# Performance work log

Measured on AMD Instinct MI355X. Metric: run time of the kernel, lower is better.

Reference implementation:

```python
import jax, jax.numpy as jnp
import numpy as np

N = 100000      # num_nodes
E = 600000      # edges per relation
R = 3           # num_relations
F_IN = 128
F_OUT = 64


def setup_inputs() -> dict:
    key = jax.random.key(0)
    k0, k1, k2, k3 = jax.random.split(key, 4)
    x = jax.random.normal(k0, (N, F_IN), dtype=jnp.float32)
    edge_indices = jax.random.randint(k1, (R, 2, E), 0, N, dtype=jnp.int32)
    # torch.randperm per relation -> fixed permutations as int inputs
    perms = jnp.stack([jax.random.permutation(jax.random.fold_in(k2, r), N).astype(jnp.int32)
                       for r in range(R)])
    # GCNConv glorot weight + zero bias, one per relation
    Ws = jax.random.normal(k3, (R, F_IN, F_OUT), dtype=jnp.float32) * (1.0 / np.sqrt(F_IN))
    bs = jnp.zeros((R, F_OUT), dtype=jnp.float32)
    return {"x": x, "edge_indices": edge_indices, "perms": perms, "Ws": Ws, "bs": bs}


def gcn_conv(h, src, dst, W, b, n):
    """PyG GCNConv: add self-loops, sym-normalize, linear, scatter-sum, bias."""
    loops = jnp.arange(n, dtype=src.dtype)
    s = jnp.concatenate([src, loops])
    d = jnp.concatenate([dst, loops])
    deg = jax.ops.segment_sum(jnp.ones_like(s, dtype=h.dtype), d, num_segments=n)
    dinv = jnp.where(deg > 0, jax.lax.rsqrt(deg), 0.0)
    norm = dinv[s] * dinv[d]                      # [E+n]
    hw = h @ W                                    # [n, F_OUT]
    out = jax.ops.segment_sum(hw[s] * norm[:, None], d, num_segments=n)
    return out + b


def reference(x, edge_indices, perms, Ws, bs):
    # Eval mode: F.dropout(p=0.5, training=False) is identity.
    n = x.shape[0]
    pos_hs, neg_hs, summaries = [], [], []
    for r in range(R):
        src, dst = edge_indices[r, 0], edge_indices[r, 1]
        pos_h = jax.nn.relu(gcn_conv(x, src, dst, Ws[r], bs[r], n))
        neg_h = jax.nn.relu(gcn_conv(x[perms[r]], src, dst, Ws[r], bs[r], n))
        pos_hs.append(pos_h)
        neg_hs.append(neg_h)
        summaries.append(pos_h.mean(axis=0, keepdims=True))
    return (jnp.stack(pos_hs), jnp.stack(neg_hs), jnp.stack(summaries))
```

## Files before the change

kernel.cpp:

```cpp
#include <hip/hip_runtime.h>

#define F_IN 128
#define F_OUT 64
#define NCHUNK 256

typedef float f32x2 __attribute__((ext_vector_type(2)));
typedef float f32x4 __attribute__((ext_vector_type(4)));
typedef short bf16x8 __attribute__((ext_vector_type(8)));

__device__ __forceinline__ unsigned short f2bf(float f) {
    unsigned int u = __float_as_uint(f);
    u += 0x7fff + ((u >> 16) & 1);
    return (unsigned short)(u >> 16);
}
__device__ __forceinline__ float bf2f(unsigned short s) {
    return __uint_as_float((unsigned int)s << 16);
}

__global__ __launch_bounds__(256) void prep_kernel(const int* __restrict__ ei,
                                                   const int* __restrict__ perm,
                                                   const float* __restrict__ W,
                                                   int* __restrict__ deg,
                                                   int* __restrict__ eoff,
                                                   int* __restrict__ ip,
                                                   unsigned short* __restrict__ wt_hi,
                                                   unsigned short* __restrict__ wt_lo,
                                                   int N, int E, int R,
                                                   int degB, int invB) {
    int b = blockIdx.x;
    if (b < degB) {
        int idx = b * 256 + threadIdx.x;
        if (idx < R * E) {
            int r = idx / E, e = idx - r * E;
            int d = ei[(size_t)r * 2 * E + E + e];
            int pos = atomicAdd(&deg[(size_t)r * N + d], 1);
            eoff[idx] = pos;
        }
    } else if (b < degB + invB) {
        int idx = (b - degB) * 256 + threadIdx.x;
        if (idx < R * N) {
            int r = idx / N, i = idx - r * N;
            ip[(size_t)r * N + perm[idx]] = i;
        }
    } else {
        int idx = (b - degB - invB) * 256 + threadIdx.x;
        if (idx < R * 64 * 128) {
            int k = idx & 127, c = (idx >> 7) & 63, r = idx >> 13;
            float v = W[((size_t)r * F_IN + k) * F_OUT + c];
            unsigned short h = f2bf(v);
            wt_hi[idx] = h;
            wt_lo[idx] = f2bf(v - bf2f(h));
        }
    }
}

__global__ __launch_bounds__(256) void scan_partial(const int* __restrict__ deg,
                                                    int* __restrict__ psum,
                                                    int N, int chunk) {
    int b = blockIdx.x;
    int r = b >> 8, c = b & 255;
    int start = c * chunk, end = min(start + chunk, N);
    int s = 0;
    for (int i = start + threadIdx.x; i < end; i += 256)
        s += deg[(size_t)r * N + i];
    __shared__ int ls[256];
    ls[threadIdx.x] = s;
    __syncthreads();
    for (int off = 128; off > 0; off >>= 1) {
        if (threadIdx.x < off) ls[threadIdx.x] += ls[threadIdx.x + off];
        __syncthreads();
    }
    if (threadIdx.x == 0) psum[b] = ls[0];
}

__global__ __launch_bounds__(256) void scan_apply2(const int* __restrict__ deg,
                                                   const int* __restrict__ psum,
                                                   int* __restrict__ rowstart,
                                                   float* __restrict__ dinv,
                                                   int N, int chunk) {
    int b = blockIdx.x;
    int r = b >> 8, c = b & 255;
    int tid = threadIdx.x, lane = tid & 63, wv = tid >> 6;
    __shared__ int incl[256];
    __shared__ int wsum[4];

    int pv = psum[(r << 8) + tid];
    int sc = pv;
    #pragma unroll
    for (int off = 1; off < 64; off <<= 1) {
        int t = __shfl_up(sc, off, 64);
        if (lane >= off) sc += t;
    }
    if (lane == 63) wsum[wv] = sc;
    __syncthreads();
    int woff = 0;
    for (int w = 0; w < wv; ++w) woff += wsum[w];
    incl[tid] = woff + sc;
    __syncthreads();
    int base = (c == 0) ? 0 : incl[c - 1];
    if (c == 0 && tid == 0)
        rowstart[(size_t)r * (N + 1) + N] = incl[255];

    int start = c * chunk, end = min(start + chunk, N);
    const int* dg = deg + (size_t)r * N;
    int* rs = rowstart + (size_t)r * (N + 1);
    float* dv = dinv + (size_t)r * N;
    int v[4]; int tsum = 0;
    #pragma unroll
    for (int j = 0; j < 4; ++j) {
        int idx = start + tid * 4 + j;
        v[j] = (idx < end) ? dg[idx] : 0;
        tsum += v[j];
    }
    int sc2 = tsum;
    #pragma unroll
    for (int off = 1; off < 64; off <<= 1) {
        int t = __shfl_up(sc2, off, 64);
        if (lane >= off) sc2 += t;
    }
    if (lane == 63) wsum[wv] = sc2;
    __syncthreads();
    int woff2 = 0;
    for (int w = 0; w < wv; ++w) woff2 += wsum[w];
    int excl = base + woff2 + sc2 - tsum;
    #pragma unroll
    for (int j = 0; j < 4; ++j) {
        int idx = start + tid * 4 + j;
        if (idx < end) {
            rs[idx] = excl;
            dv[idx] = rsqrtf((float)(v[j] + 1));
        }
        excl += v[j];
    }
}

__global__ __launch_bounds__(256) void gemm_xw(const float* __restrict__ x,
                                               const unsigned short* __restrict__ wt_hi,
                                               const unsigned short* __restrict__ wt_lo,
                                               const int* __restrict__ ip,
                                               unsigned short* __restrict__ combined,
                                               int N, int R) {
    constexpr int KP = 136;
    __shared__ __align__(16) unsigned short xs_hi[64 * KP];
    __shared__ __align__(16) unsigned short xs_lo[64 * KP];

    int row0 = blockIdx.x * 64;
    int tid = threadIdx.x;
    {
        int rr = tid >> 2, q = tid & 3;
        int grow = row0 + rr; if (grow >= N) grow = N - 1;
        const float* xr = x + (size_t)grow * F_IN + q * 32;
        unsigned short* dh = &xs_hi[rr * KP + q * 32];
        unsigned short* dl = &xs_lo[rr * KP + q * 32];
        #pragma unroll
        for (int c = 0; c < 32; c += 4) {
            float4 v = *(const float4*)(xr + c);
            unsigned short h0 = f2bf(v.x), h1 = f2bf(v.y),
                           h2 = f2bf(v.z), h3 = f2bf(v.w);
            ushort4 hv; hv.x = h0; hv.y = h1; hv.z = h2; hv.w = h3;
            *(ushort4*)(dh + c) = hv;
            ushort4 lv;
            lv.x = f2bf(v.x - bf2f(h0)); lv.y = f2bf(v.y - bf2f(h1));
            lv.z = f2bf(v.z - bf2f(h2)); lv.w = f2bf(v.w - bf2f(h3));
            *(ushort4*)(dl + c) = lv;
        }
    }
    __syncthreads();

    int wv = tid >> 6, lane = tid & 63;
    int l15 = lane & 15, lhi = lane >> 4;
    int nbase = wv * 16;
    for (int r = 0; r < R; ++r) {
        f32x4 acc[4];
        #pragma unroll
        for (int ct = 0; ct < 4; ++ct) acc[ct] = (f32x4){0.f, 0.f, 0.f, 0.f};
        const unsigned short* wh = wt_hi + (size_t)r * 64 * 128;
        const unsigned short* wl = wt_lo + (size_t)r * 64 * 128;
        #pragma unroll
        for (int kc = 0; kc < 4; ++kc) {
            int kb = kc * 32 + lhi * 8;
            int ro = (nbase + l15) * KP + kb;
            bf16x8 bh = *(const bf16x8*)&xs_hi[ro];
            bf16x8 bl = *(const bf16x8*)&xs_lo[ro];
            bf16x8 ah[4], al[4];
            #pragma unroll
            for (int ct = 0; ct < 4; ++ct) {
                int wo = (ct * 16 + l15) * 128 + kb;
                ah[ct] = *(const bf16x8*)(wh + wo);
                al[ct] = *(const bf16x8*)(wl + wo);
            }
            #pragma unroll
            for (int ct = 0; ct < 4; ++ct) {
                acc[ct] = __builtin_amdgcn_mfma_f32_16x16x32_bf16(ah[ct], bh, acc[ct], 0, 0, 0);
                acc[ct] = __builtin_amdgcn_mfma_f32_16x16x32_bf16(ah[ct], bl, acc[ct], 0, 0, 0);
                acc[ct] = __builtin_amdgcn_mfma_f32_16x16x32_bf16(al[ct], bh, acc[ct], 0, 0, 0);
            }
        }
        const int* ipr = ip + (size_t)r * N;
        size_t rb = (size_t)r * N;
        int xrow = row0 + nbase + l15;
        if (xrow < N) {
            int nrow = ipr[xrow];
            #pragma unroll
            for (int ct = 0; ct < 4; ++ct) {
                f32x4 a = acc[ct];
                ushort4 v;
                v.x = f2bf(a.x); v.y = f2bf(a.y);
                v.z = f2bf(a.z); v.w = f2bf(a.w);
                int cb = ct * 16 + lhi * 4;
                *(ushort4*)(combined + (rb + xrow) * 128 + cb) = v;
                *(ushort4*)(combined + (rb + nrow) * 128 + 64 + cb) = v;
            }
        }
    }
}

__global__ __launch_bounds__(256) void fill_csr2(const int* __restrict__ ei,
                                                 const int* __restrict__ eoff,
                                                 const int* __restrict__ rowstart,
                                                 const float* __restrict__ dinv,
                                                 int2* __restrict__ csr,
                                                 int N, int E, int R) {
    int idx = blockIdx.x * 256 + threadIdx.x;
    if (idx >= R * E) return;
    int r = idx / E, e = idx - r * E;
    const int* base = ei + (size_t)r * 2 * E;
    int s = base[e], d = base[E + e];
    const float* dv = dinv + (size_t)r * N;
    float nrm = dv[s] * dv[d];
    int pos = rowstart[(size_t)r * (N + 1) + d] + eoff[idx];
    int2 sp; sp.x = s; sp.y = __float_as_int(nrm);
    csr[(size_t)r * E + pos] = sp;
}

__global__ __launch_bounds__(256) void gather_kernel(const int2* __restrict__ csr,
                                                     const int* __restrict__ rowstart,
                                                     const float* __restrict__ dinv,
                                                     const unsigned short* __restrict__ combined,
                                                     const float* __restrict__ bs,
                                                     float* __restrict__ out_pos,
                                                     float* __restrict__ out_neg,
                                                     float* __restrict__ partial,
                                                     int N, int E, int perRel) {
    int bid = blockIdx.x;
    int r = bid / perRel, ib = bid - r * perRel;
    int lane = threadIdx.x & 63, wv = threadIdx.x >> 6;
    int i = ib * 4 + wv;
    i = __builtin_amdgcn_readfirstlane(i);
    int c0 = (lane & 31) * 2;
    __shared__ float ls[4][64];
    float p0 = 0.f, p1 = 0.f;
    if (i < N) {
        const unsigned short* cw = combined + (size_t)r * N * 128;
        const int* rs = rowstart + (size_t)r * (N + 1);
        int j0 = rs[i], j1 = rs[i + 1];
        j0 = __builtin_amdgcn_readfirstlane(j0);
        j1 = __builtin_amdgcn_readfirstlane(j1);
        float di = dinv[(size_t)r * N + i];
        float w = di * di;
        unsigned int sv = *(const unsigned int*)(cw + (size_t)i * 128 + 2 * lane);
        float acc0 = bf2f((unsigned short)sv) * w;
        float acc1 = bf2f((unsigned short)(sv >> 16)) * w;
        const int2* cs = csr + (size_t)r * E;
        int last = j1 - 1;
        for (int j = j0; j < j1; j += 8) {
            int2 e[8];
            float nm[8];
            #pragma unroll
            for (int k = 0; k < 8; ++k) {
                int idx = j + k;
                int ic = idx < last ? idx : last;
                e[k] = cs[ic];
                nm[k] = (idx < j1) ? __int_as_float(e[k].y) : 0.f;
            }
            #pragma unroll
            for (int k = 0; k < 8; ++k) {
                unsigned int v = *(const unsigned int*)(cw + (size_t)e[k].x * 128 + 2 * lane);
                acc0 += bf2f((unsigned short)v) * nm[k];
                acc1 += bf2f((unsigned short)(v >> 16)) * nm[k];
            }
        }
        float2 bv = *(const float2*)(bs + r * F_OUT + c0);
        float q0 = acc0 + bv.x; q0 = q0 > 0.f ? q0 : 0.f;
        float q1 = acc1 + bv.y; q1 = q1 > 0.f ? q1 : 0.f;
        size_t off = (size_t)r * N * F_OUT + (size_t)i * F_OUT + c0;
        float* dst = (lane < 32) ? (out_pos + off) : (out_neg + off);
        f32x2 o; o.x = q0; o.y = q1;
        __builtin_nontemporal_store(o, (f32x2*)dst);
        if (lane < 32) { p0 = q0; p1 = q1; }
    }
    if (lane < 32) { ls[wv][c0] = p0; ls[wv][c0 + 1] = p1; }
    __syncthreads();
    if (wv == 0) {
        float t = ls[0][lane] + ls[1][lane] + ls[2][lane] + ls[3][lane];
        atomicAdd(&partial[((size_t)r * 256 + (ib & 255)) * F_OUT + lane], t);
    }
}

__global__ __launch_bounds__(256) void summary_reduce(const float* __restrict__ partial,
                                                      float* __restrict__ summary,
                                                      float inv_n) {
    int r = blockIdx.x;
    int lane = threadIdx.x & 63, wv = threadIdx.x >> 6;
    __shared__ float ls[256];
    float s = 0.f;
    for (int c = wv; c < 256; c += 4)
        s += partial[((size_t)r * 256 + c) * F_OUT + lane];
    ls[threadIdx.x] = s;
    __syncthreads();
    if (wv == 0)
        summary[r * F_OUT + lane] =
            (ls[lane] + ls[64 + lane] + ls[128 + lane] + ls[192 + lane]) * inv_n;
}

extern "C" void kernel_launch(void* const* d_in, const int* in_sizes, int n_in,
                              void* d_out, int out_size, void* d_ws, size_t ws_size,
                              hipStream_t stream) {
    const float* x    = (const float*)d_in[0];
    const int*   ei   = (const int*)d_in[1];
    const int*   perm = (const int*)d_in[2];
    const float* Ws   = (const float*)d_in[3];
    const float* bs   = (const float*)d_in[4];

    const int N = in_sizes[0] / F_IN;
    const int R = in_sizes[4] / F_OUT;
    const int E = in_sizes[1] / (2 * R);

    float* out_pos = (float*)d_out;
    float* out_neg = out_pos + (size_t)R * N * F_OUT;
    float* summary = out_neg + (size_t)R * N * F_OUT;

    char* ws = (char*)d_ws;
    size_t off = 0;
    auto alloc = [&](size_t bytes) { void* p = ws + off;
        off += (bytes + 255) & ~(size_t)255; return p; };
    int*   deg      = (int*)  alloc((size_t)R * N * 4);
    float* partial  = (float*)alloc((size_t)R * 256 * F_OUT * 4);
    float* dinv     = (float*)alloc((size_t)R * N * 4);
    int*   rowstart = (int*)  alloc((size_t)R * (N + 1) * 4);
    int*   ip       = (int*)  alloc((size_t)R * N * 4);
    int*   eoff     = (int*)  alloc((size_t)R * E * 4);
    int2*  csr      = (int2*) alloc((size_t)R * E * 8);
    unsigned short* combined = (unsigned short*)alloc((size_t)R * N * 128 * 2);
    int*   psum     = (int*)  alloc((size_t)R * NCHUNK * 4);
    unsigned short* wt_hi = (unsigned short*)alloc((size_t)R * 64 * 128 * 2);
    unsigned short* wt_lo = (unsigned short*)alloc((size_t)R * 64 * 128 * 2);

    const int chunk = (N + NCHUNK - 1) / NCHUNK;
    const int degB = (R * E + 255) / 256;
    const int invB = (R * N + 255) / 256;
    const int wB   = (R * 64 * 128 + 255) / 256;
    const int gemmB = (N + 63) / 64;
    const int perRel = (N + 3) / 4;

    size_t zbytes = (size_t)((char*)dinv - (char*)deg);
    hipMemsetAsync(deg, 0, zbytes, stream);

    prep_kernel<<<degB + invB + wB, 256, 0, stream>>>(ei, perm, Ws, deg, eoff,
                                                      ip, wt_hi, wt_lo, N, E, R,
                                                      degB, invB);
    scan_partial<<<R * NCHUNK, 256, 0, stream>>>(deg, psum, N, chunk);
    scan_apply2<<<R * NCHUNK, 256, 0, stream>>>(deg, psum, rowstart, dinv, N, chunk);
    gemm_xw<<<gemmB, 256, 0, stream>>>(x, wt_hi, wt_lo, ip, combined, N, R);
    fill_csr2<<<(R * E + 255) / 256, 256, 0, stream>>>(ei, eoff, rowstart, dinv,
                                                       csr, N, E, R);
    gather_kernel<<<perRel * R, 256, 0, stream>>>(csr, rowstart, dinv, combined,
                                                  bs, out_pos, out_neg, partial,
                                                  N, E, perRel);
    summary_reduce<<<R, 256, 0, stream>>>(partial, summary, 1.0f / (float)N);
}
```

Baseline: 529.6 us.

## Drop permuted combined buffer; gather negatives via permuted source indices in CSR

The GEMM now writes a single bf16 hw table per relation instead of a combined buffer holding both the identity and inverse-permuted copies, and the inverse-permutation pass is removed. The CSR entries grow to int4 so each edge carries both the source index and perm[source]; the upper half-wave gathers negative-branch rows through the permuted index. The gather kernel also handles two destination rows per wave to raise memory-level parallelism. This halves GEMM output writes and the footprint of the gathered table, but doubles CSR bytes and makes each half-wave read separate 128-byte rows, so gathers become less coalesced.

```diff
diff --git a/kernel.cpp b/kernel.cpp
--- a/kernel.cpp
+++ b/kernel.cpp
@@ -18,15 +18,12 @@
 }
 
 __global__ __launch_bounds__(256) void prep_kernel(const int* __restrict__ ei,
-                                                   const int* __restrict__ perm,
                                                    const float* __restrict__ W,
                                                    int* __restrict__ deg,
                                                    int* __restrict__ eoff,
-                                                   int* __restrict__ ip,
                                                    unsigned short* __restrict__ wt_hi,
                                                    unsigned short* __restrict__ wt_lo,
-                                                   int N, int E, int R,
-                                                   int degB, int invB) {
+                                                   int N, int E, int R, int degB) {
     int b = blockIdx.x;
     if (b < degB) {
         int idx = b * 256 + threadIdx.x;
@@ -36,14 +33,8 @@
             int pos = atomicAdd(&deg[(size_t)r * N + d], 1);
             eoff[idx] = pos;
         }
-    } else if (b < degB + invB) {
+    } else {
         int idx = (b - degB) * 256 + threadIdx.x;
-        if (idx < R * N) {
-            int r = idx / N, i = idx - r * N;
-            ip[(size_t)r * N + perm[idx]] = i;
-        }
-    } else {
-        int idx = (b - degB - invB) * 256 + threadIdx.x;
         if (idx < R * 64 * 128) {
             int k = idx & 127, c = (idx >> 7) & 63, r = idx >> 13;
             float v = W[((size_t)r * F_IN + k) * F_OUT + c];
@@ -137,8 +128,7 @@
 __global__ __launch_bounds__(256) void gemm_xw(const float* __restrict__ x,
                                                const unsigned short* __restrict__ wt_hi,
                                                const unsigned short* __restrict__ wt_lo,
-                                               const int* __restrict__ ip,
-                                               unsigned short* __restrict__ combined,
+                                               unsigned short* __restrict__ hw,
                                                int N, int R) {
     constexpr int KP = 136;
     __shared__ __align__(16) unsigned short xs_hi[64 * KP];
@@ -196,11 +186,9 @@
                 acc[ct] = __builtin_amdgcn_mfma_f32_16x16x32_bf16(al[ct], bh, acc[ct], 0, 0, 0);
             }
         }
-        const int* ipr = ip + (size_t)r * N;
         size_t rb = (size_t)r * N;
         int xrow = row0 + nbase + l15;
         if (xrow < N) {
-            int nrow = ipr[xrow];
             #pragma unroll
             for (int ct = 0; ct < 4; ++ct) {
                 f32x4 a = acc[ct];
@@ -208,18 +196,18 @@
                 v.x = f2bf(a.x); v.y = f2bf(a.y);
                 v.z = f2bf(a.z); v.w = f2bf(a.w);
                 int cb = ct * 16 + lhi * 4;
-                *(ushort4*)(combined + (rb + xrow) * 128 + cb) = v;
-                *(ushort4*)(combined + (rb + nrow) * 128 + 64 + cb) = v;
-            }
-        }
-    }
-}
-
-__global__ __launch_bounds__(256) void fill_csr2(const int* __restrict__ ei,
+                *(ushort4*)(hw + (rb + xrow) * 64 + cb) = v;
+            }
+        }
+    }
+}
+
+__global__ __launch_bounds__(256) void fill_csr3(const int* __restrict__ ei,
                                                  const int* __restrict__ eoff,
                                                  const int* __restrict__ rowstart,
                                                  const float* __restrict__ dinv,
-                                                 int2* __restrict__ csr,
+                                                 const int* __restrict__ perm,
+                                                 int4* __restrict__ csr,
                                                  int N, int E, int R) {
     int idx = blockIdx.x * 256 + threadIdx.x;
     if (idx >= R * E) return;
@@ -228,15 +216,17 @@
     int s = base[e], d = base[E + e];
     const float* dv = dinv + (size_t)r * N;
     float nrm = dv[s] * dv[d];
+    int ps = perm[(size_t)r * N + s];
     int pos = rowstart[(size_t)r * (N + 1) + d] + eoff[idx];
-    int2 sp; sp.x = s; sp.y = __float_as_int(nrm);
+    int4 sp; sp.x = s; sp.y = ps; sp.z = __float_as_int(nrm); sp.w = 0;
     csr[(size_t)r * E + pos] = sp;
 }
 
-__global__ __launch_bounds__(256) void gather_kernel(const int2* __restrict__ csr,
+__global__ __launch_bounds__(256) void gather_kernel(const int4* __restrict__ csr,
                                                      const int* __restrict__ rowstart,
                                                      const float* __restrict__ dinv,
-                                                     const unsigned short* __restrict__ combined,
+                                                     const unsigned short* __restrict__ hw,
+                                                     const int* __restrict__ perm,
                                                      const float* __restrict__ bs,
                                                      float* __restrict__ out_pos,
                                                      float* __restrict__ out_neg,
@@ -245,49 +235,69 @@
     int bid = blockIdx.x;
     int r = bid / perRel, ib = bid - r * perRel;
     int lane = threadIdx.x & 63, wv = threadIdx.x >> 6;
-    int i = ib * 4 + wv;
-    i = __builtin_amdgcn_readfirstlane(i);
+    int i0 = __builtin_amdgcn_readfirstlane(ib * 8 + wv * 2);
+    int half = lane >> 5;
     int c0 = (lane & 31) * 2;
     __shared__ float ls[4][64];
+    const unsigned short* hwr = hw + (size_t)r * N * 64;
+    const int* rs = rowstart + (size_t)r * (N + 1);
+    const float* dv = dinv + (size_t)r * N;
+    const int* pm = perm + (size_t)r * N;
+    const int4* cs = csr + (size_t)r * E;
     float p0 = 0.f, p1 = 0.f;
-    if (i < N) {
-        const unsigned short* cw = combined + (size_t)r * N * 128;
-        const int* rs = rowstart + (size_t)r * (N + 1);
-        int j0 = rs[i], j1 = rs[i + 1];
-        j0 = __builtin_amdgcn_readfirstlane(j0);
-        j1 = __builtin_amdgcn_readfirstlane(j1);
-        float di = dinv[(size_t)r * N + i];
-        float w = di * di;
-        unsigned int sv = *(const unsigned int*)(cw + (size_t)i * 128 + 2 * lane);
-        float acc0 = bf2f((unsigned short)sv) * w;
-        float acc1 = bf2f((unsigned short)(sv >> 16)) * w;
-        const int2* cs = csr + (size_t)r * E;
-        int last = j1 - 1;
-        for (int j = j0; j < j1; j += 8) {
-            int2 e[8];
-            float nm[8];
+    int nrows = (i0 < N) ? min(2, N - i0) : 0;
+    float acc0[2] = {0.f, 0.f}, acc1[2] = {0.f, 0.f};
+    int j[2] = {0, 0}, jend[2] = {0, 0};
+    float w[2] = {0.f, 0.f};
+    int selfrow[2] = {0, 0};
+    for (int q = 0; q < nrows; ++q) {
+        int i = i0 + q;
+        j[q]    = __builtin_amdgcn_readfirstlane(rs[i]);
+        jend[q] = __builtin_amdgcn_readfirstlane(rs[i + 1]);
+        float di = dv[i]; w[q] = di * di;
+        int pi = __builtin_amdgcn_readfirstlane(pm[i]);
+        selfrow[q] = half ? pi : i;
+    }
+    for (int q = 0; q < nrows; ++q) {
+        unsigned int sv = *(const unsigned int*)(hwr + (size_t)selfrow[q] * 64 + c0);
+        acc0[q] += bf2f((unsigned short)sv) * w[q];
+        acc1[q] += bf2f((unsigned short)(sv >> 16)) * w[q];
+    }
+    while (j[0] < jend[0] || j[1] < jend[1]) {
+        int esrc[2][8]; float enm[2][8];
+        #pragma unroll
+        for (int q = 0; q < 2; ++q) {
+            bool act = j[q] < jend[q];
+            int base = act ? j[q] : 0;
+            int last = act ? jend[q] - 1 : 0;
             #pragma unroll
             for (int k = 0; k < 8; ++k) {
-                int idx = j + k;
+                int idx = base + k;
                 int ic = idx < last ? idx : last;
-                e[k] = cs[ic];
-                nm[k] = (idx < j1) ? __int_as_float(e[k].y) : 0.f;
-            }
+                int4 e = cs[ic];
+                esrc[q][k] = half ? e.y : e.x;
+                enm[q][k] = (act && idx < jend[q]) ? __int_as_float(e.z) : 0.f;
+            }
+            if (act) j[q] += 8;
+        }
+        #pragma unroll
+        for (int q = 0; q < 2; ++q)
             #pragma unroll
             for (int k = 0; k < 8; ++k) {
-                unsigned int v = *(const unsigned int*)(cw + (size_t)e[k].x * 128 + 2 * lane);
-                acc0 += bf2f((unsigned short)v) * nm[k];
-                acc1 += bf2f((unsigned short)(v >> 16)) * nm[k];
-            }
-        }
-        float2 bv = *(const float2*)(bs + r * F_OUT + c0);
-        float q0 = acc0 + bv.x; q0 = q0 > 0.f ? q0 : 0.f;
-        float q1 = acc1 + bv.y; q1 = q1 > 0.f ? q1 : 0.f;
-        size_t off = (size_t)r * N * F_OUT + (size_t)i * F_OUT + c0;
+                unsigned int v = *(const unsigned int*)(hwr + (size_t)esrc[q][k] * 64 + c0);
+                acc0[q] += bf2f((unsigned short)v) * enm[q][k];
+                acc1[q] += bf2f((unsigned short)(v >> 16)) * enm[q][k];
+            }
+    }
+    const float2 bv = *(const float2*)(bs + r * F_OUT + c0);
+    for (int q = 0; q < nrows; ++q) {
+        float q0 = acc0[q] + bv.x; q0 = q0 > 0.f ? q0 : 0.f;
+        float q1 = acc1[q] + bv.y; q1 = q1 > 0.f ? q1 : 0.f;
+        size_t off = (size_t)r * N * F_OUT + (size_t)(i0 + q) * F_OUT + c0;
         float* dst = (lane < 32) ? (out_pos + off) : (out_neg + off);
         f32x2 o; o.x = q0; o.y = q1;
         __builtin_nontemporal_store(o, (f32x2*)dst);
-        if (lane < 32) { p0 = q0; p1 = q1; }
+        if (lane < 32) { p0 += q0; p1 += q1; }
     }
     if (lane < 32) { ls[wv][c0] = p0; ls[wv][c0 + 1] = p1; }
     __syncthreads();
@@ -338,33 +348,29 @@
     float* partial  = (float*)alloc((size_t)R * 256 * F_OUT * 4);
     float* dinv     = (float*)alloc((size_t)R * N * 4);
     int*   rowstart = (int*)  alloc((size_t)R * (N + 1) * 4);
-    int*   ip       = (int*)  alloc((size_t)R * N * 4);
     int*   eoff     = (int*)  alloc((size_t)R * E * 4);
-    int2*  csr      = (int2*) alloc((size_t)R * E * 8);
-    unsigned short* combined = (unsigned short*)alloc((size_t)R * N * 128 * 2);
+    int4*  csr      = (int4*) alloc((size_t)R * E * 16);
+    unsigned short* hw = (unsigned short*)alloc((size_t)R * N * 64 * 2);
     int*   psum     = (int*)  alloc((size_t)R * NCHUNK * 4);
     unsigned short* wt_hi = (unsigned short*)alloc((size_t)R * 64 * 128 * 2);
     unsigned short* wt_lo = (unsigned short*)alloc((size_t)R * 64 * 128 * 2);
 
     const int chunk = (N + NCHUNK - 1) / NCHUNK;
     const int degB = (R * E + 255) / 256;
-    const int invB = (R * N + 255) / 256;
     const int wB   = (R * 64 * 128 + 255) / 256;
     const int gemmB = (N + 63) / 64;
-    const int perRel = (N + 3) / 4;
+    const int perRel = (N + 7) / 8;
 
     size_t zbytes = (size_t)((char*)dinv - (char*)deg);
     hipMemsetAsync(deg, 0, zbytes, stream);
 
-    prep_kernel<<<degB + invB + wB, 256, 0, stream>>>(ei, perm, Ws, deg, eoff,
-                                                      ip, wt_hi, wt_lo, N, E, R,
-                                                      degB, invB);
+    prep_kernel<<<degB + wB, 256, 0, stream>>>(ei, Ws, deg, eoff, wt_hi, wt_lo,
+                                               N, E, R, degB);
     scan_partial<<<R * NCHUNK, 256, 0, stream>>>(deg, psum, N, chunk);
     scan_apply2<<<R * NCHUNK, 256, 0, stream>>>(deg, psum, rowstart, dinv, N, chunk);
-    gemm_xw<<<gemmB, 256, 0, stream>>>(x, wt_hi, wt_lo, ip, combined, N, R);
-    fill_csr2<<<(R * E + 255) / 256, 256, 0, stream>>>(ei, eoff, rowstart, dinv,
-                                                       csr, N, E, R);
-    gather_kernel<<<perRel * R, 256, 0, stream>>>(csr, rowstart, dinv, combined,
+    gemm_xw<<<gemmB, 256, 0, stream>>>(x, wt_hi, wt_lo, hw, N, R);
+    fill_csr3<<<degB, 256, 0, stream>>>(ei, eoff, rowstart, dinv, perm, csr, N, E, R);
+    gather_kernel<<<perRel * R, 256, 0, stream>>>(csr, rowstart, dinv, hw, perm,
                                                   bs, out_pos, out_neg, partial,
                                                   N, E, perRel);
     summary_reduce<<<R, 256, 0, stream>>>(partial, summary, 1.0f / (float)N);
```

Result: no change. 536.3 us (+1.3%).
